# Kernel optimization log

Hardware: AMD Instinct MI355X
Metric: run time of the kernel (lower is better)

The kernel has to match this reference:

```python
import jax, jax.numpy as jnp
import numpy as np

B, L, EMB, H, NL, E, MAXA, PAD = 64, 512, 400, 256, 3, 512, 32, 0


def setup_inputs() -> dict:
    key = jax.random.key(0)
    ks = jax.random.split(key, 12)
    s = lambda k, shape: jax.random.normal(k, shape, jnp.float32) * 0.02
    Semb = jax.random.normal(ks[0], (B, EMB, L), jnp.float32)
    word_ids = jax.random.randint(ks[1], (B, L), 0, 30000)
    y1 = jax.random.randint(ks[2], (B,), 0, L - MAXA)
    span = jax.random.randint(ks[3], (B,), 0, MAXA)
    y2 = y1 + span
    edges = jax.random.randint(ks[4], (B, E, 2), 0, L)
    return dict(
        Semb=Semb,
        ans_sent_word_ids=word_ids,
        y1_in_sent=y1,
        y2_in_sent=y2,
        edges=edges,
        W1=s(ks[5], (H, EMB)),                 # Initialized_Conv1d (k=1, no bias)
        hw_lin_W=s(ks[6], (2, H, H)), hw_lin_b=jnp.zeros((2, H), jnp.float32),
        hw_gate_W=s(ks[7], (2, H, H)), hw_gate_b=jnp.zeros((2, H), jnp.float32),
        gcn_W=s(ks[8], (NL, H, H)), gcn_b=jnp.zeros((NL, H), jnp.float32),
        conv_W=s(ks[9], (1, NL * H)), conv_b=jnp.zeros((1,), jnp.float32),
        lin_W=s(ks[10], (L, L)), lin_b=jnp.zeros((L,), jnp.float32),
    )


def reference(Semb, ans_sent_word_ids, y1_in_sent, y2_in_sent, edges,
              W1, hw_lin_W, hw_lin_b, hw_gate_W, hw_gate_b,
              gcn_W, gcn_b, conv_W, conv_b, lin_W, lin_b):
    # 1x1 conv: [B, EMB, L] -> [B, H, L]
    x = jnp.einsum('oi,bit->bot', W1, Semb)
    # 2-layer Highway (dropout is identity in eval)
    for i in range(2):
        gate = jax.nn.sigmoid(jnp.einsum('oi,bit->bot', hw_gate_W[i], x) + hw_gate_b[i][None, :, None])
        nonlin = jnp.einsum('oi,bit->bot', hw_lin_W[i], x) + hw_lin_b[i][None, :, None]
        x = gate * nonlin + (1.0 - gate) * x
    maskS = (ans_sent_word_ids != PAD).astype(x.dtype)            # [B, L]
    # answer-span mask (Aemb itself is dead code in the original forward's output)
    pos = y1_in_sent[:, None] + jnp.arange(MAXA)                   # [B, MAXA]
    maskA = (pos <= y2_in_sent[:, None]).astype(x.dtype)
    # dense adjacency from edge list (undirected since gcn_directed=False)
    bidx = jnp.broadcast_to(jnp.arange(B)[:, None], (B, E))
    adj = jnp.zeros((B, L, L), x.dtype)
    adj = adj.at[bidx, edges[..., 0], edges[..., 1]].set(1.0)
    adj = adj.at[bidx, edges[..., 1], edges[..., 0]].set(1.0)
    # GCN (C-GCN style: W(Ax) + W(x), note bias counted twice, /(deg+1), relu)
    h = x.transpose(0, 2, 1)                                       # [B, L, H]
    denom = jnp.sum(adj, axis=2, keepdims=True) + 1.0              # [B, L, 1]
    outs = []
    for l in range(NL):
        Ax = jnp.einsum('bls,bsh->blh', adj, h)
        AxW = jnp.einsum('blh,oh->blo', Ax + h, gcn_W[l]) + 2.0 * gcn_b[l]
        h = jax.nn.relu(AxW / denom)
        outs.append(h)
    cat = jnp.concatenate(outs, axis=2)                            # [B, L, NL*H]
    y = jax.nn.relu(jnp.einsum('blc,oc->bol', cat, conv_W) + conv_b[None, :, None])  # [B,1,L]
    logits = (jnp.einsum('bol,ml->bom', y, lin_W) + lin_b).squeeze(1)                # [B,L]
    logits = logits * maskS + (1.0 - maskS) * (-1e30)
    return (logits, maskA)
```

## Files before the change

### kernel.cpp

```cpp
#include <hip/hip_runtime.h>
#include <cstdint>

#define B 64
#define L 512
#define EMB 400
#define KPAD 416
#define H 256
#define NL 3
#define NE 512
#define MAXA 32
#define M_TOT (B * L)

typedef unsigned short u16;
typedef float f32x4 __attribute__((ext_vector_type(4)));
typedef short short8 __attribute__((ext_vector_type(8)));
typedef u16 u16x8 __attribute__((ext_vector_type(8)));

__device__ __forceinline__ float b2f(u16 u) {
  unsigned v = ((unsigned)u) << 16;
  return __builtin_bit_cast(float, v);
}
__device__ __forceinline__ u16 f2b(float f) {
  unsigned u = __builtin_bit_cast(unsigned, f);
  unsigned r = (u + 0x7fffu + ((u >> 16) & 1u)) >> 16;
  return (u16)r;
}

#define GL16(g, l)                                                              \
  __builtin_amdgcn_global_load_lds((const __attribute__((address_space(1))) void*)(g), \
                                   (__attribute__((address_space(3))) void*)(l), 16, 0, 0)

template <int EPI>
__global__ __launch_bounds__(256, 2) void gemm128(const u16* __restrict__ A,
                                                  const u16* __restrict__ Bw,
                                                  const u16* __restrict__ B2w, int K,
                                                  const float* __restrict__ bias1,
                                                  const float* __restrict__ bias2,
                                                  const u16* __restrict__ Xres,
                                                  const float* __restrict__ rden,
                                                  const float* __restrict__ cw,
                                                  float* __restrict__ yv,
                                                  u16* __restrict__ Out) {
  __shared__ u16 Al[128 * 32];
  __shared__ u16 Bl[128 * 32];
  __shared__ u16 Cl[128 * 32];

  const int t = threadIdx.x;
  const int wid = t >> 6, lane = t & 63;
  const int wm = wid >> 1, wn = wid & 1;
  const int m0 = blockIdx.x * 128, n0 = blockIdx.y * 128;

  const int r4 = t >> 2, kseg = t & 3;
  u16* alb1 = Al + (size_t)(wid * 64) * 8;
  u16* alb2 = Al + (size_t)(256 + wid * 64) * 8;
  u16* blb1 = Bl + (size_t)(wid * 64) * 8;
  u16* blb2 = Bl + (size_t)(256 + wid * 64) * 8;
  u16* clb1 = Cl + (size_t)(wid * 64) * 8;
  u16* clb2 = Cl + (size_t)(256 + wid * 64) * 8;

  f32x4 acc[4][4] = {};
  f32x4 acc2[4][4] = {};

  const int fr = lane & 15, kg = lane >> 4;
  const int nk = K >> 5;

  for (int kk = 0; kk < nk; ++kk) {
    const int k0 = kk * 32;
    {
      const u16* ga = A + (size_t)(m0 + r4) * K + k0 + kseg * 8;
      GL16(ga, alb1);
      GL16(ga + (size_t)64 * K, alb2);
      const u16* gb = Bw + (size_t)(n0 + r4) * K + k0 + kseg * 8;
      GL16(gb, blb1);
      GL16(gb + (size_t)64 * K, blb2);
      if constexpr (EPI == 1) {
        const u16* gc = B2w + (size_t)(n0 + r4) * K + k0 + kseg * 8;
        GL16(gc, clb1);
        GL16(gc + (size_t)64 * K, clb2);
      }
    }
    __syncthreads();

    short8 af[4], bf[4], cf[4];
#pragma unroll
    for (int i = 0; i < 4; ++i) {
      af[i] = *(const short8*)(Al + ((size_t)(wm * 64 + i * 16 + fr) * 4 + kg) * 8);
      bf[i] = *(const short8*)(Bl + ((size_t)(wn * 64 + i * 16 + fr) * 4 + kg) * 8);
      if constexpr (EPI == 1)
        cf[i] = *(const short8*)(Cl + ((size_t)(wn * 64 + i * 16 + fr) * 4 + kg) * 8);
    }
#pragma unroll
    for (int mi = 0; mi < 4; ++mi)
#pragma unroll
      for (int ni = 0; ni < 4; ++ni) {
        acc[mi][ni] = __builtin_amdgcn_mfma_f32_16x16x32_bf16(af[mi], bf[ni], acc[mi][ni], 0, 0, 0);
        if constexpr (EPI == 1)
          acc2[mi][ni] =
              __builtin_amdgcn_mfma_f32_16x16x32_bf16(af[mi], cf[ni], acc2[mi][ni], 0, 0, 0);
      }
    __syncthreads();
  }

  const int r0 = m0 + wm * 64 + kg * 4;
  const int c0 = n0 + wn * 64 + fr;
  float ypart[16];
  if constexpr (EPI == 2) {
#pragma unroll
    for (int q = 0; q < 16; ++q) ypart[q] = 0.f;
  }
#pragma unroll
  for (int ni = 0; ni < 4; ++ni) {
    const int col = c0 + ni * 16;
    float b1 = 0.f, b2 = 0.f, cwv = 0.f;
    if constexpr (EPI == 1) { b1 = bias1[col]; b2 = bias2[col]; }
    if constexpr (EPI == 2) { b1 = 2.f * bias1[col]; cwv = cw[col]; }
#pragma unroll
    for (int mi = 0; mi < 4; ++mi) {
#pragma unroll
      for (int r = 0; r < 4; ++r) {
        const int row = r0 + mi * 16 + r;
        const float v = acc[mi][ni][r];
        if constexpr (EPI == 0) {
          Out[(size_t)row * H + col] = f2b(v);
        } else if constexpr (EPI == 1) {
          const float g = 1.f / (1.f + __expf(-(v + b1)));
          const float nn = acc2[mi][ni][r] + b2;
          const float x = b2f(Xres[(size_t)row * H + col]);
          Out[(size_t)row * H + col] = f2b(g * nn + (1.f - g) * x);
        } else {
          const float s = (v + b1) * rden[row];
          const float rl = s > 0.f ? s : 0.f;
          ypart[mi * 4 + r] += rl * cwv;
          Out[(size_t)row * H + col] = f2b(rl);
        }
      }
    }
  }
  if constexpr (EPI == 2) {
#pragma unroll
    for (int q = 0; q < 16; ++q) {
      float p = ypart[q];
      p += __shfl_xor(p, 1);
      p += __shfl_xor(p, 2);
      p += __shfl_xor(p, 4);
      p += __shfl_xor(p, 8);
      if (fr == 0) atomicAdd(&yv[r0 + (q >> 2) * 16 + (q & 3)], p);
    }
  }
}

__global__ __launch_bounds__(256) void k_sembT(const float* __restrict__ Semb,
                                               u16* __restrict__ A0) {
  const int b = blockIdx.x, e0 = blockIdx.y * 64, l0 = blockIdx.z * 64;
  __shared__ u16 tile[64][72];
  const int t = threadIdx.x;
  {
    const int er = t >> 2, ls = (t & 3) * 16;
    if (e0 + er < EMB) {
      const float* src = Semb + ((size_t)b * EMB + e0 + er) * L + l0 + ls;
#pragma unroll
      for (int i = 0; i < 4; ++i) {
        const float4 v = *(const float4*)(src + i * 4);
        tile[er][ls + i * 4 + 0] = f2b(v.x);
        tile[er][ls + i * 4 + 1] = f2b(v.y);
        tile[er][ls + i * 4 + 2] = f2b(v.z);
        tile[er][ls + i * 4 + 3] = f2b(v.w);
      }
    } else {
#pragma unroll
      for (int i = 0; i < 16; ++i) tile[er][ls + i] = 0;
    }
  }
  __syncthreads();
  {
    const int lr = t >> 2, es = (t & 3) * 16;
    if (e0 + es < KPAD) {
      u16x8 v0, v1;
#pragma unroll
      for (int i = 0; i < 8; ++i) v0[i] = tile[es + i][lr];
#pragma unroll
      for (int i = 0; i < 8; ++i) v1[i] = tile[es + 8 + i][lr];
      u16* dst = A0 + (size_t)(b * L + l0 + lr) * KPAD + e0 + es;
      *(u16x8*)dst = v0;
      *(u16x8*)(dst + 8) = v1;
    }
  }
}

__global__ void k_cvt(const float* __restrict__ in, u16* __restrict__ out, int n) {
  const int i = blockIdx.x * 256 + threadIdx.x;
  if (i < n) out[i] = f2b(in[i]);
}

__global__ void k_cvt_w1(const float* __restrict__ W1, u16* __restrict__ out) {
  const int i = blockIdx.x * 256 + threadIdx.x;
  const int o = i / KPAD, k = i - o * KPAD;
  out[i] = (k < EMB) ? f2b(W1[o * EMB + k]) : (u16)0;
}

__global__ void k_edges(const int* __restrict__ edges, unsigned* __restrict__ bm) {
  const int t = blockIdx.x * 256 + threadIdx.x;
  const int b = t >> 9, e = t & 511;
  const int u = edges[(size_t)(b * NE + e) * 2 + 0];
  const int v = edges[(size_t)(b * NE + e) * 2 + 1];
  atomicOr(&bm[(size_t)(b * L + u) * 16 + (v >> 5)], 1u << (v & 31));
  atomicOr(&bm[(size_t)(b * L + v) * 16 + (u >> 5)], 1u << (u & 31));
}

__global__ void k_rden(const unsigned* __restrict__ bm, float* __restrict__ rden) {
  const int m = blockIdx.x * 256 + threadIdx.x;
  const uint4* p = (const uint4*)(bm + (size_t)m * 16);
  int c = 0;
#pragma unroll
  for (int w = 0; w < 4; ++w) {
    const uint4 v = p[w];
    c += __popc(v.x) + __popc(v.y) + __popc(v.z) + __popc(v.w);
  }
  rden[m] = 1.f / (1.f + (float)c);
}

__global__ __launch_bounds__(256) void k_gather(const unsigned* __restrict__ bm,
                                                const u16* __restrict__ h,
                                                u16* __restrict__ T) {
  const int t = threadIdx.x;
  const int tok = blockIdx.x * 8 + (t >> 5);
  const int b = tok >> 9;
  const int c = (t & 31) * 8;
  const uint4* wp4 = (const uint4*)(bm + (size_t)tok * 16);
  const uint4 w0 = wp4[0], w1 = wp4[1], w2 = wp4[2], w3 = wp4[3];
  const unsigned wa[16] = {w0.x, w0.y, w0.z, w0.w, w1.x, w1.y, w1.z, w1.w,
                           w2.x, w2.y, w2.z, w2.w, w3.x, w3.y, w3.z, w3.w};
  float acc[8];
  {
    const u16x8 v = *(const u16x8*)(h + (size_t)tok * H + c);
#pragma unroll
    for (int i = 0; i < 8; ++i) acc[i] = b2f(v[i]);
  }
#pragma unroll
  for (int wi = 0; wi < 16; ++wi) {
    unsigned bits = wa[wi];
    while (bits) {
      const int bit = __ffs(bits) - 1;
      bits &= bits - 1;
      const int s = wi * 32 + bit;
      const u16x8 u = *(const u16x8*)(h + (size_t)(b * L + s) * H + c);
#pragma unroll
      for (int i = 0; i < 8; ++i) acc[i] += b2f(u[i]);
    }
  }
  u16x8 o;
#pragma unroll
  for (int i = 0; i < 8; ++i) o[i] = f2b(acc[i]);
  *(u16x8*)(T + (size_t)tok * H + c) = o;
}

__global__ __launch_bounds__(256) void k_logits(const float* __restrict__ yv,
                                                const float* __restrict__ cb,
                                                const float* __restrict__ lw,
                                                const float* __restrict__ lb,
                                                const int* __restrict__ wids,
                                                float* __restrict__ out) {
  const int b = blockIdx.x >> 1;
  const int m = ((blockIdx.x & 1) << 8) + threadIdx.x;
  __shared__ float ys[512];
  const float cb0 = cb[0];
  ys[threadIdx.x] = fmaxf(yv[(size_t)b * L + threadIdx.x] + cb0, 0.f);
  ys[threadIdx.x + 256] = fmaxf(yv[(size_t)b * L + 256 + threadIdx.x] + cb0, 0.f);
  __syncthreads();
  float acc = lb[m];
  const float4* wr = (const float4*)(lw + (size_t)m * L);
#pragma unroll 4
  for (int l4 = 0; l4 < 128; ++l4) {
    const float4 w4 = wr[l4];
    acc += ys[l4 * 4] * w4.x + ys[l4 * 4 + 1] * w4.y + ys[l4 * 4 + 2] * w4.z +
           ys[l4 * 4 + 3] * w4.w;
  }
  out[(size_t)b * L + m] = (wids[(size_t)b * L + m] != 0) ? acc : -1.0e30f;
}

__global__ void k_maskA(const int* __restrict__ y1, const int* __restrict__ y2,
                        float* __restrict__ out) {
  const int t = blockIdx.x * 256 + threadIdx.x;
  const int b = t >> 5, j = t & 31;
  out[t] = (y1[b] + j <= y2[b]) ? 1.0f : 0.0f;
}

extern "C" void kernel_launch(void* const* d_in, const int* in_sizes, int n_in,
                              void* d_out, int out_size, void* d_ws, size_t ws_size,
                              hipStream_t stream) {
  (void)in_sizes; (void)n_in; (void)out_size; (void)ws_size;
  const float* Semb      = (const float*)d_in[0];
  const int*   wids      = (const int*)d_in[1];
  const int*   y1        = (const int*)d_in[2];
  const int*   y2        = (const int*)d_in[3];
  const int*   edges     = (const int*)d_in[4];
  const float* W1        = (const float*)d_in[5];
  const float* hw_lin_W  = (const float*)d_in[6];
  const float* hw_lin_b  = (const float*)d_in[7];
  const float* hw_gate_W = (const float*)d_in[8];
  const float* hw_gate_b = (const float*)d_in[9];
  const float* gcn_W     = (const float*)d_in[10];
  const float* gcn_b     = (const float*)d_in[11];
  const float* conv_W    = (const float*)d_in[12];
  const float* conv_b    = (const float*)d_in[13];
  const float* lin_W     = (const float*)d_in[14];
  const float* lin_b     = (const float*)d_in[15];
  float* out = (float*)d_out;

  char* ws = (char*)d_ws;
  const size_t SZA = (size_t)M_TOT * KPAD * 2;
  const size_t SZX = (size_t)M_TOT * H * 2;
  u16* A0   = (u16*)(ws);
  u16* P0b  = (u16*)(ws + SZA);
  u16* P1b  = (u16*)(ws + SZA + SZX);
  u16* O0   = (u16*)(ws + SZA + 2 * SZX);
  u16* O1   = (u16*)(ws + SZA + 3 * SZX);
  u16* O2   = (u16*)(ws + SZA + 4 * SZX);
  char* wp  = ws + SZA + 5 * SZX;
  u16* W1b  = (u16*)(wp);
  u16* HWGb = (u16*)(wp + 212992);
  u16* HWLb = (u16*)(wp + 212992 + 262144);
  u16* GCNb = (u16*)(wp + 212992 + 2 * 262144);
  char* sp  = wp + 212992 + 2 * 262144 + 393216;
  unsigned* bm   = (unsigned*)(sp);
  float*    yv   = (float*)(sp + 2097152);
  float*    rden = (float*)(sp + 2097152 + 131072);

  hipMemsetAsync(bm, 0, 2097152 + 131072, stream);
  k_edges<<<dim3(B * NE / 256), 256, 0, stream>>>(edges, bm);
  k_rden<<<dim3(B * L / 256), 256, 0, stream>>>(bm, rden);

  k_cvt_w1<<<dim3(256 * KPAD / 256), 256, 0, stream>>>(W1, W1b);
  k_cvt<<<dim3(2 * H * H / 256), 256, 0, stream>>>(hw_gate_W, HWGb, 2 * H * H);
  k_cvt<<<dim3(2 * H * H / 256), 256, 0, stream>>>(hw_lin_W, HWLb, 2 * H * H);
  k_cvt<<<dim3(NL * H * H / 256), 256, 0, stream>>>(gcn_W, GCNb, NL * H * H);
  k_sembT<<<dim3(B, 7, 8), 256, 0, stream>>>(Semb, A0);

  gemm128<0><<<dim3(M_TOT / 128, 2), 256, 0, stream>>>(A0, W1b, nullptr, KPAD, nullptr, nullptr,
                                                       nullptr, nullptr, nullptr, nullptr, P0b);
  gemm128<1><<<dim3(M_TOT / 128, 2), 256, 0, stream>>>(P0b, HWGb, HWLb, H, hw_gate_b, hw_lin_b,
                                                       P0b, nullptr, nullptr, nullptr, P1b);
  gemm128<1><<<dim3(M_TOT / 128, 2), 256, 0, stream>>>(P1b, HWGb + H * H, HWLb + H * H, H,
                                                       hw_gate_b + H, hw_lin_b + H, P1b, nullptr,
                                                       nullptr, nullptr, P0b);
  const u16* hin = P0b;
  u16* outs[3] = {O0, O1, O2};
  for (int l = 0; l < NL; ++l) {
    k_gather<<<dim3(M_TOT / 8), 256, 0, stream>>>(bm, hin, P1b);
    gemm128<2><<<dim3(M_TOT / 128, 2), 256, 0, stream>>>(P1b, GCNb + l * H * H, nullptr, H,
                                                         gcn_b + l * H, nullptr, nullptr, rden,
                                                         conv_W + l * H, yv, outs[l]);
    hin = outs[l];
  }

  k_logits<<<dim3(B * 2), 256, 0, stream>>>(yv, conv_b, lin_W, lin_b, wids, out);
  k_maskA<<<dim3(B * MAXA / 256), 256, 0, stream>>>(y1, y2, out + B * L);
}
```

Baseline: 193.7 us.

## Fuse GCN neighbor gather into 64-row full-width GEMM and merge small kernels

The GEMM is retiled to 64 rows by the full 256 output columns per block. The GCN adjacency gather now runs inside the GEMM's A-tile load, which removes the separate gather kernel and its intermediate buffer round trip. The highway residual is now read from a shared-memory copy of the A tile instead of from global memory, and the last GCN layer skips writing its output. The weight conversions and maskA are merged into single launches. In exchange, the gather's irregular loads now sit on the GEMM's critical path and stall the MFMA loop, and the larger shared-memory footprint may reduce occupancy.

Measured after the change: 290.6 us. +50.0%, slower.

```diff
diff --git a/kernel.cpp b/kernel.cpp
--- a/kernel.cpp
+++ b/kernel.cpp
@@ -31,112 +31,146 @@
                                    (__attribute__((address_space(3))) void*)(l), 16, 0, 0)
 
 template <int EPI>
-__global__ __launch_bounds__(256, 2) void gemm128(const u16* __restrict__ A,
-                                                  const u16* __restrict__ Bw,
-                                                  const u16* __restrict__ B2w, int K,
-                                                  const float* __restrict__ bias1,
-                                                  const float* __restrict__ bias2,
-                                                  const u16* __restrict__ Xres,
-                                                  const float* __restrict__ rden,
-                                                  const float* __restrict__ cw,
-                                                  float* __restrict__ yv,
-                                                  u16* __restrict__ Out) {
-  __shared__ u16 Al[128 * 32];
-  __shared__ u16 Bl[128 * 32];
-  __shared__ u16 Cl[128 * 32];
+__global__ __launch_bounds__(256, 2) void gemm64(
+    const u16* __restrict__ A, const u16* __restrict__ Bw, const u16* __restrict__ B2w,
+    const int K,
+    const float* __restrict__ bias1, const float* __restrict__ bias2,
+    const unsigned* __restrict__ bmp, const float* __restrict__ rden,
+    const float* __restrict__ cw, float* __restrict__ yv, u16* __restrict__ Out) {
+  constexpr bool HW = (EPI == 1);
+  constexpr bool GCN = (EPI >= 2);
+  __shared__ u16 Al[64 * 32];
+  __shared__ u16 Bl[256 * 32];
+  __shared__ u16 Cl[HW ? 256 * 32 : 8];
+  __shared__ u16 Xl[HW ? 64 * 256 : 8];
 
   const int t = threadIdx.x;
   const int wid = t >> 6, lane = t & 63;
-  const int wm = wid >> 1, wn = wid & 1;
-  const int m0 = blockIdx.x * 128, n0 = blockIdx.y * 128;
-
-  const int r4 = t >> 2, kseg = t & 3;
-  u16* alb1 = Al + (size_t)(wid * 64) * 8;
-  u16* alb2 = Al + (size_t)(256 + wid * 64) * 8;
-  u16* blb1 = Bl + (size_t)(wid * 64) * 8;
-  u16* blb2 = Bl + (size_t)(256 + wid * 64) * 8;
-  u16* clb1 = Cl + (size_t)(wid * 64) * 8;
-  u16* clb2 = Cl + (size_t)(256 + wid * 64) * 8;
+  const int m0 = blockIdx.x * 64;
+  const int fr = lane & 15, kg = lane >> 4;
+  const int r4 = t >> 2, ksg = t & 3;
+  const int bb = m0 >> 9;
+
+  unsigned bmv[16];
+  if constexpr (GCN) {
+    const unsigned* p = bmp + (size_t)(m0 + r4) * 16;
+#pragma unroll
+    for (int i = 0; i < 16; ++i) bmv[i] = p[i];
+  }
 
   f32x4 acc[4][4] = {};
   f32x4 acc2[4][4] = {};
 
-  const int fr = lane & 15, kg = lane >> 4;
   const int nk = K >> 5;
-
   for (int kk = 0; kk < nk; ++kk) {
-    const int k0 = kk * 32;
-    {
-      const u16* ga = A + (size_t)(m0 + r4) * K + k0 + kseg * 8;
-      GL16(ga, alb1);
-      GL16(ga + (size_t)64 * K, alb2);
-      const u16* gb = Bw + (size_t)(n0 + r4) * K + k0 + kseg * 8;
-      GL16(gb, blb1);
-      GL16(gb + (size_t)64 * K, blb2);
-      if constexpr (EPI == 1) {
-        const u16* gc = B2w + (size_t)(n0 + r4) * K + k0 + kseg * 8;
-        GL16(gc, clb1);
-        GL16(gc + (size_t)64 * K, clb2);
+    const int kc = kk * 32 + ksg * 8;
+#pragma unroll
+    for (int c = 0; c < 4; ++c)
+      GL16(Bw + (size_t)(c * 64 + r4) * K + kc, Bl + (size_t)(c * 256 + wid * 64) * 8);
+    if constexpr (HW) {
+#pragma unroll
+      for (int c = 0; c < 4; ++c)
+        GL16(B2w + (size_t)(c * 64 + r4) * K + kc, Cl + (size_t)(c * 256 + wid * 64) * 8);
+    }
+    if constexpr (!GCN) {
+      GL16(A + (size_t)(m0 + r4) * K + kc, Al + (size_t)(wid * 64) * 8);
+    } else {
+      float a[8];
+      const u16x8 v = *(const u16x8*)(A + (size_t)(m0 + r4) * H + kc);
+#pragma unroll
+      for (int i = 0; i < 8; ++i) a[i] = b2f(v[i]);
+#pragma unroll
+      for (int wi = 0; wi < 16; ++wi) {
+        unsigned bits = bmv[wi];
+        while (bits) {
+          const int bit = __ffs(bits) - 1;
+          bits &= bits - 1;
+          const u16x8 u = *(const u16x8*)(A + (size_t)(bb * L + wi * 32 + bit) * H + kc);
+#pragma unroll
+          for (int i = 0; i < 8; ++i) a[i] += b2f(u[i]);
+        }
       }
+      u16x8 o;
+#pragma unroll
+      for (int i = 0; i < 8; ++i) o[i] = f2b(a[i]);
+      *(u16x8*)(Al + (size_t)t * 8) = o;
     }
     __syncthreads();
 
+    if constexpr (HW) {
+      const u16x8 xv = *(const u16x8*)(Al + (size_t)t * 8);
+      *(u16x8*)(Xl + (size_t)(kk * 256 + t) * 8) = xv;
+    }
+
     short8 af[4], bf[4], cf[4];
 #pragma unroll
     for (int i = 0; i < 4; ++i) {
-      af[i] = *(const short8*)(Al + ((size_t)(wm * 64 + i * 16 + fr) * 4 + kg) * 8);
-      bf[i] = *(const short8*)(Bl + ((size_t)(wn * 64 + i * 16 + fr) * 4 + kg) * 8);
-      if constexpr (EPI == 1)
-        cf[i] = *(const short8*)(Cl + ((size_t)(wn * 64 + i * 16 + fr) * 4 + kg) * 8);
+      af[i] = *(const short8*)(Al + ((size_t)(i * 16 + fr) * 4 + kg) * 8);
+      bf[i] = *(const short8*)(Bl + ((size_t)(wid * 64 + i * 16 + fr) * 4 + kg) * 8);
+      if constexpr (HW)
+        cf[i] = *(const short8*)(Cl + ((size_t)(wid * 64 + i * 16 + fr) * 4 + kg) * 8);
     }
 #pragma unroll
     for (int mi = 0; mi < 4; ++mi)
 #pragma unroll
       for (int ni = 0; ni < 4; ++ni) {
         acc[mi][ni] = __builtin_amdgcn_mfma_f32_16x16x32_bf16(af[mi], bf[ni], acc[mi][ni], 0, 0, 0);
-        if constexpr (EPI == 1)
+        if constexpr (HW)
           acc2[mi][ni] =
               __builtin_amdgcn_mfma_f32_16x16x32_bf16(af[mi], cf[ni], acc2[mi][ni], 0, 0, 0);
       }
     __syncthreads();
   }
 
-  const int r0 = m0 + wm * 64 + kg * 4;
-  const int c0 = n0 + wn * 64 + fr;
-  float ypart[16];
-  if constexpr (EPI == 2) {
+  const int r0 = kg * 4;
+  const int c0 = wid * 64 + fr;
+  if constexpr (EPI == 0) {
+#pragma unroll
+    for (int ni = 0; ni < 4; ++ni) {
+      const int col = c0 + ni * 16;
+#pragma unroll
+      for (int mi = 0; mi < 4; ++mi)
+#pragma unroll
+        for (int rr = 0; rr < 4; ++rr)
+          Out[(size_t)(m0 + mi * 16 + r0 + rr) * H + col] = f2b(acc[mi][ni][rr]);
+    }
+  } else if constexpr (EPI == 1) {
+#pragma unroll
+    for (int ni = 0; ni < 4; ++ni) {
+      const int col = c0 + ni * 16;
+      const float b1 = bias1[col], b2 = bias2[col];
+      const int xbase = (col >> 5) * 2048 + (col & 31);
+#pragma unroll
+      for (int mi = 0; mi < 4; ++mi)
+#pragma unroll
+        for (int rr = 0; rr < 4; ++rr) {
+          const int rl = mi * 16 + r0 + rr;
+          const float g = 1.f / (1.f + __expf(-(acc[mi][ni][rr] + b1)));
+          const float nn = acc2[mi][ni][rr] + b2;
+          const float x = b2f(Xl[xbase + rl * 32]);
+          Out[(size_t)(m0 + rl) * H + col] = f2b(g * nn + (1.f - g) * x);
+        }
+    }
+  } else {
+    float ypart[16];
 #pragma unroll
     for (int q = 0; q < 16; ++q) ypart[q] = 0.f;
-  }
-#pragma unroll
-  for (int ni = 0; ni < 4; ++ni) {
-    const int col = c0 + ni * 16;
-    float b1 = 0.f, b2 = 0.f, cwv = 0.f;
-    if constexpr (EPI == 1) { b1 = bias1[col]; b2 = bias2[col]; }
-    if constexpr (EPI == 2) { b1 = 2.f * bias1[col]; cwv = cw[col]; }
-#pragma unroll
-    for (int mi = 0; mi < 4; ++mi) {
-#pragma unroll
-      for (int r = 0; r < 4; ++r) {
-        const int row = r0 + mi * 16 + r;
-        const float v = acc[mi][ni][r];
-        if constexpr (EPI == 0) {
-          Out[(size_t)row * H + col] = f2b(v);
-        } else if constexpr (EPI == 1) {
-          const float g = 1.f / (1.f + __expf(-(v + b1)));
-          const float nn = acc2[mi][ni][r] + b2;
-          const float x = b2f(Xres[(size_t)row * H + col]);
-          Out[(size_t)row * H + col] = f2b(g * nn + (1.f - g) * x);
-        } else {
-          const float s = (v + b1) * rden[row];
+#pragma unroll
+    for (int ni = 0; ni < 4; ++ni) {
+      const int col = c0 + ni * 16;
+      const float b1 = 2.f * bias1[col];
+      const float cwv = cw[col];
+#pragma unroll
+      for (int mi = 0; mi < 4; ++mi)
+#pragma unroll
+        for (int rr = 0; rr < 4; ++rr) {
+          const int row = m0 + mi * 16 + r0 + rr;
+          const float s = (acc[mi][ni][rr] + b1) * rden[row];
           const float rl = s > 0.f ? s : 0.f;
-          ypart[mi * 4 + r] += rl * cwv;
-          Out[(size_t)row * H + col] = f2b(rl);
+          ypart[mi * 4 + rr] += rl * cwv;
+          if constexpr (EPI == 2) Out[(size_t)row * H + col] = f2b(rl);
         }
-      }
-    }
-  }
-  if constexpr (EPI == 2) {
+    }
 #pragma unroll
     for (int q = 0; q < 16; ++q) {
       float p = ypart[q];
@@ -144,7 +178,7 @@
       p += __shfl_xor(p, 2);
       p += __shfl_xor(p, 4);
       p += __shfl_xor(p, 8);
-      if (fr == 0) atomicAdd(&yv[r0 + (q >> 2) * 16 + (q & 3)], p);
+      if (fr == 0) atomicAdd(&yv[m0 + (q >> 2) * 16 + r0 + (q & 3)], p);
     }
   }
 }
@@ -187,15 +221,22 @@
   }
 }
 
-__global__ void k_cvt(const float* __restrict__ in, u16* __restrict__ out, int n) {
-  const int i = blockIdx.x * 256 + threadIdx.x;
-  if (i < n) out[i] = f2b(in[i]);
-}
-
-__global__ void k_cvt_w1(const float* __restrict__ W1, u16* __restrict__ out) {
-  const int i = blockIdx.x * 256 + threadIdx.x;
-  const int o = i / KPAD, k = i - o * KPAD;
-  out[i] = (k < EMB) ? f2b(W1[o * EMB + k]) : (u16)0;
+__global__ void k_cvtall(const float* __restrict__ W1, const float* __restrict__ gW,
+                         const float* __restrict__ lW, const float* __restrict__ gcnW,
+                         u16* __restrict__ W1b, u16* __restrict__ HWGb,
+                         u16* __restrict__ HWLb, u16* __restrict__ GCNb) {
+  int i = blockIdx.x * 256 + threadIdx.x;
+  if (i < 256 * KPAD) {
+    const int o = i / KPAD, k = i - o * KPAD;
+    W1b[i] = (k < EMB) ? f2b(W1[o * EMB + k]) : (u16)0;
+    return;
+  }
+  i -= 256 * KPAD;
+  if (i < 2 * H * H) { HWGb[i] = f2b(gW[i]); return; }
+  i -= 2 * H * H;
+  if (i < 2 * H * H) { HWLb[i] = f2b(lW[i]); return; }
+  i -= 2 * H * H;
+  if (i < NL * H * H) GCNb[i] = f2b(gcnW[i]);
 }
 
 __global__ void k_edges(const int* __restrict__ edges, unsigned* __restrict__ bm) {
@@ -219,47 +260,23 @@
   rden[m] = 1.f / (1.f + (float)c);
 }
 
-__global__ __launch_bounds__(256) void k_gather(const unsigned* __restrict__ bm,
-                                                const u16* __restrict__ h,
-                                                u16* __restrict__ T) {
-  const int t = threadIdx.x;
-  const int tok = blockIdx.x * 8 + (t >> 5);
-  const int b = tok >> 9;
-  const int c = (t & 31) * 8;
-  const uint4* wp4 = (const uint4*)(bm + (size_t)tok * 16);
-  const uint4 w0 = wp4[0], w1 = wp4[1], w2 = wp4[2], w3 = wp4[3];
-  const unsigned wa[16] = {w0.x, w0.y, w0.z, w0.w, w1.x, w1.y, w1.z, w1.w,
-                           w2.x, w2.y, w2.z, w2.w, w3.x, w3.y, w3.z, w3.w};
-  float acc[8];
-  {
-    const u16x8 v = *(const u16x8*)(h + (size_t)tok * H + c);
-#pragma unroll
-    for (int i = 0; i < 8; ++i) acc[i] = b2f(v[i]);
-  }
-#pragma unroll
-  for (int wi = 0; wi < 16; ++wi) {
-    unsigned bits = wa[wi];
-    while (bits) {
-      const int bit = __ffs(bits) - 1;
-      bits &= bits - 1;
-      const int s = wi * 32 + bit;
-      const u16x8 u = *(const u16x8*)(h + (size_t)(b * L + s) * H + c);
-#pragma unroll
-      for (int i = 0; i < 8; ++i) acc[i] += b2f(u[i]);
-    }
-  }
-  u16x8 o;
-#pragma unroll
-  for (int i = 0; i < 8; ++i) o[i] = f2b(acc[i]);
-  *(u16x8*)(T + (size_t)tok * H + c) = o;
-}
-
 __global__ __launch_bounds__(256) void k_logits(const float* __restrict__ yv,
                                                 const float* __restrict__ cb,
                                                 const float* __restrict__ lw,
                                                 const float* __restrict__ lb,
                                                 const int* __restrict__ wids,
+                                                const int* __restrict__ y1,
+                                                const int* __restrict__ y2,
                                                 float* __restrict__ out) {
+  if (blockIdx.x == B * 2) {
+#pragma unroll
+    for (int j = 0; j < 8; ++j) {
+      const int idx = j * 256 + threadIdx.x;
+      const int b = idx >> 5, q = idx & 31;
+      out[B * L + idx] = (y1[b] + q <= y2[b]) ? 1.0f : 0.0f;
+    }
+    return;
+  }
   const int b = blockIdx.x >> 1;
   const int m = ((blockIdx.x & 1) << 8) + threadIdx.x;
   __shared__ float ys[512];
@@ -276,13 +293,6 @@
            ys[l4 * 4 + 3] * w4.w;
   }
   out[(size_t)b * L + m] = (wids[(size_t)b * L + m] != 0) ? acc : -1.0e30f;
-}
-
-__global__ void k_maskA(const int* __restrict__ y1, const int* __restrict__ y2,
-                        float* __restrict__ out) {
-  const int t = blockIdx.x * 256 + threadIdx.x;
-  const int b = t >> 5, j = t & 31;
-  out[t] = (y1[b] + j <= y2[b]) ? 1.0f : 0.0f;
 }
 
 extern "C" void kernel_launch(void* const* d_in, const int* in_sizes, int n_in,
@@ -315,8 +325,7 @@
   u16* P1b  = (u16*)(ws + SZA + SZX);
   u16* O0   = (u16*)(ws + SZA + 2 * SZX);
   u16* O1   = (u16*)(ws + SZA + 3 * SZX);
-  u16* O2   = (u16*)(ws + SZA + 4 * SZX);
-  char* wp  = ws + SZA + 5 * SZX;
+  char* wp  = ws + SZA + 4 * SZX;
   u16* W1b  = (u16*)(wp);
   u16* HWGb = (u16*)(wp + 212992);
   u16* HWLb = (u16*)(wp + 212992 + 262144);
@@ -330,29 +339,24 @@
   k_edges<<<dim3(B * NE / 256), 256, 0, stream>>>(edges, bm);
   k_rden<<<dim3(B * L / 256), 256, 0, stream>>>(bm, rden);
 
-  k_cvt_w1<<<dim3(256 * KPAD / 256), 256, 0, stream>>>(W1, W1b);
-  k_cvt<<<dim3(2 * H * H / 256), 256, 0, stream>>>(hw_gate_W, HWGb, 2 * H * H);
-  k_cvt<<<dim3(2 * H * H / 256), 256, 0, stream>>>(hw_lin_W, HWLb, 2 * H * H);
-  k_cvt<<<dim3(NL * H * H / 256), 256, 0, stream>>>(gcn_W, GCNb, NL * H * H);
+  k_cvtall<<<dim3((256 * KPAD + 4 * H * H + NL * H * H + 255) / 256), 256, 0, stream>>>(
+      W1, hw_gate_W, hw_lin_W, gcn_W, W1b, HWGb, HWLb, GCNb);
   k_sembT<<<dim3(B, 7, 8), 256, 0, stream>>>(Semb, A0);
 
-  gemm128<0><<<dim3(M_TOT / 128, 2), 256, 0, stream>>>(A0, W1b, nullptr, KPAD, nullptr, nullptr,
-                                                       nullptr, nullptr, nullptr, nullptr, P0b);
-  gemm128<1><<<dim3(M_TOT / 128, 2), 256, 0, stream>>>(P0b, HWGb, HWLb, H, hw_gate_b, hw_lin_b,
-                                                       P0b, nullptr, nullptr, nullptr, P1b);
-  gemm128<1><<<dim3(M_TOT / 128, 2), 256, 0, stream>>>(P1b, HWGb + H * H, HWLb + H * H, H,
-                                                       hw_gate_b + H, hw_lin_b + H, P1b, nullptr,
-                                                       nullptr, nullptr, P0b);
-  const u16* hin = P0b;
-  u16* outs[3] = {O0, O1, O2};
-  for (int l = 0; l < NL; ++l) {
-    k_gather<<<dim3(M_TOT / 8), 256, 0, stream>>>(bm, hin, P1b);
-    gemm128<2><<<dim3(M_TOT / 128, 2), 256, 0, stream>>>(P1b, GCNb + l * H * H, nullptr, H,
-                                                         gcn_b + l * H, nullptr, nullptr, rden,
-                                                         conv_W + l * H, yv, outs[l]);
-    hin = outs[l];
-  }
-
-  k_logits<<<dim3(B * 2), 256, 0, stream>>>(yv, conv_b, lin_W, lin_b, wids, out);
-  k_maskA<<<dim3(B * MAXA / 256), 256, 0, stream>>>(y1, y2, out + B * L);
-}
+  gemm64<0><<<dim3(M_TOT / 64), 256, 0, stream>>>(A0, W1b, nullptr, KPAD, nullptr, nullptr,
+                                                  nullptr, nullptr, nullptr, nullptr, P0b);
+  gemm64<1><<<dim3(M_TOT / 64), 256, 0, stream>>>(P0b, HWGb, HWLb, H, hw_gate_b, hw_lin_b,
+                                                  nullptr, nullptr, nullptr, nullptr, P1b);
+  gemm64<1><<<dim3(M_TOT / 64), 256, 0, stream>>>(P1b, HWGb + H * H, HWLb + H * H, H,
+                                                  hw_gate_b + H, hw_lin_b + H, nullptr, nullptr,
+                                                  nullptr, nullptr, P0b);
+  gemm64<2><<<dim3(M_TOT / 64), 256, 0, stream>>>(P0b, GCNb, nullptr, H, gcn_b, nullptr,
+                                                  bm, rden, conv_W, yv, O0);
+  gemm64<2><<<dim3(M_TOT / 64), 256, 0, stream>>>(O0, GCNb + H * H, nullptr, H, gcn_b + H,
+                                                  nullptr, bm, rden, conv_W + H, yv, O1);
+  gemm64<3><<<dim3(M_TOT / 64), 256, 0, stream>>>(O1, GCNb + 2 * H * H, nullptr, H,
+                                                  gcn_b + 2 * H, nullptr, bm, rden,
+                                                  conv_W + 2 * H, yv, nullptr);
+
+  k_logits<<<dim3(B * 2 + 1), 256, 0, stream>>>(yv, conv_b, lin_W, lin_b, wids, y1, y2, out);
+}
```
